# Optimization experiments

Measured on AMD Instinct MI355X. Metric: run time of the kernel, lower is better.

The kernel has to match this reference:

```python
import jax, jax.numpy as jnp
import numpy as np

N, E, G = 50000, 800000, 64   # nodes, edges, graphs
IN, HID, H = 128, 64, 4       # in_channels, hidden_channels, heads


def setup_inputs() -> dict:
    key = jax.random.key(0)
    ks = jax.random.split(key, 32)
    r = lambda i, shape, sc=0.05: jax.random.normal(ks[i], shape, jnp.float32) * sc
    inp = {
        "x": jax.random.normal(ks[0], (N, IN), jnp.float32),
        "edge_index": jax.random.randint(ks[1], (2, E), 0, N),
        "batch": jnp.sort(jax.random.randint(ks[2], (N,), 0, G)),
        # GATConv 1: in -> hidden, heads=4, concat
        "W1": r(3, (IN, H * HID)), "a_src1": r(4, (H, HID)), "a_dst1": r(5, (H, HID)), "b1": r(6, (H * HID,)),
        "bn1_g": 1.0 + r(7, (H * HID,)), "bn1_b": r(8, (H * HID,)), "bn1_m": r(9, (H * HID,)),
        "bn1_v": jax.random.uniform(ks[10], (H * HID,), jnp.float32, 0.5, 1.5),
        # GATConv 2: hidden*heads -> hidden, heads=4, concat
        "W2": r(11, (H * HID, H * HID)), "a_src2": r(12, (H, HID)), "a_dst2": r(13, (H, HID)), "b2": r(14, (H * HID,)),
        "bn2_g": 1.0 + r(15, (H * HID,)), "bn2_b": r(16, (H * HID,)), "bn2_m": r(17, (H * HID,)),
        "bn2_v": jax.random.uniform(ks[18], (H * HID,), jnp.float32, 0.5, 1.5),
        # GATConv 3: hidden*heads -> hidden, heads=1
        "W3": r(19, (H * HID, HID)), "a_src3": r(20, (1, HID)), "a_dst3": r(21, (1, HID)), "b3": r(22, (HID,)),
        # projection MLP: Linear(2*hidden, hidden) -> ReLU -> Linear(hidden, hidden)
        "P1": r(23, (2 * HID, HID)), "pb1": r(24, (HID,)),
        "P2": r(25, (HID, HID)), "pb2": r(26, (HID,)),
    }
    return inp


def _gat_conv(x, src, dst, n, W, a_s, a_d, b, concat):
    """PyG-style GATConv (eval mode). src/dst already include self-loops."""
    Hh, C = a_s.shape
    h = (x @ W).reshape(n, Hh, C)                       # [N, H, C]
    al_s = jnp.einsum('nhc,hc->nh', h, a_s)             # [N, H]
    al_d = jnp.einsum('nhc,hc->nh', h, a_d)             # [N, H]
    e = jax.nn.leaky_relu(al_s[src] + al_d[dst], 0.2)   # [E', H]
    # segment softmax over incoming edges of each dst node
    m = jax.ops.segment_max(e, dst, num_segments=n)     # [N, H] (finite: self-loops)
    ex = jnp.exp(e - m[dst])
    den = jax.ops.segment_sum(ex, dst, num_segments=n)
    alpha = ex / den[dst]                               # [E', H]
    out = jax.ops.segment_sum(h[src] * alpha[..., None], dst, num_segments=n)  # [N, H, C]
    out = out.reshape(n, Hh * C) if concat else out.mean(axis=1)
    return out + b


def _bn(x, g, b, m, v):
    return (x - m) * jax.lax.rsqrt(v + 1e-5) * g + b


def _forward(x, edge_index, batch,
             W1, a_src1, a_dst1, b1, bn1_g, bn1_b, bn1_m, bn1_v,
             W2, a_src2, a_dst2, b2, bn2_g, bn2_b, bn2_m, bn2_v,
             W3, a_src3, a_dst3, b3, P1, pb1, P2, pb2):
    n = x.shape[0]
    loop = jnp.arange(n)
    src = jnp.concatenate([edge_index[0], loop])        # add_self_loops=True
    dst = jnp.concatenate([edge_index[1], loop])
    h = _gat_conv(x, src, dst, n, W1, a_src1, a_dst1, b1, True)
    h = jax.nn.elu(_bn(h, bn1_g, bn1_b, bn1_m, bn1_v))  # dropout inactive in eval
    h = _gat_conv(h, src, dst, n, W2, a_src2, a_dst2, b2, True)
    h = jax.nn.elu(_bn(h, bn2_g, bn2_b, bn2_m, bn2_v))
    h = _gat_conv(h, src, dst, n, W3, a_src3, a_dst3, b3, False)  # heads=1
    x_max = jax.ops.segment_max(h, batch, num_segments=G)
    cnt = jax.ops.segment_sum(jnp.ones((n, 1), h.dtype), batch, num_segments=G)
    x_mean = jax.ops.segment_sum(h, batch, num_segments=G) / jnp.maximum(cnt, 1.0)
    z = jnp.concatenate([x_max, x_mean], axis=1)        # [G, 2*HID]
    z = jax.nn.relu(z @ P1 + pb1)
    return z @ P2 + pb2                                  # [G, HID]


def reference(x, edge_index, batch,
              W1, a_src1, a_dst1, b1, bn1_g, bn1_b, bn1_m, bn1_v,
              W2, a_src2, a_dst2, b2, bn2_g, bn2_b, bn2_m, bn2_v,
              W3, a_src3, a_dst3, b3, P1, pb1, P2, pb2):
    return _forward(x, edge_index, batch,
                    W1, a_src1, a_dst1, b1, bn1_g, bn1_b, bn1_m, bn1_v,
                    W2, a_src2, a_dst2, b2, bn2_g, bn2_b, bn2_m, bn2_v,
                    W3, a_src3, a_dst3, b3, P1, pb1, P2, pb2)
```

## Files before the change

kernel.cpp:

```cpp
#include <hip/hip_runtime.h>

typedef unsigned int uint;
typedef unsigned short ushort;

#define NFIX 50000
#define EFIX 800000
#define GFIX 64
#define BCAP 64
#define DCAP 128
#define WSTRIDE 136
#define PSL 16

__device__ __forceinline__ float bflo(uint u) { return __uint_as_float(u << 16); }
__device__ __forceinline__ float bfhi(uint u) { return __uint_as_float(u & 0xffff0000u); }
__device__ __forceinline__ float bf1(ushort u) { return __uint_as_float(((uint)u) << 16); }
__device__ __forceinline__ ushort f2bf(float f) {
    uint u = __float_as_uint(f);
    u += 0x7fffu + ((u >> 16) & 1u);
    return (ushort)(u >> 16);
}
__device__ __forceinline__ float lrelu(float x) { return fmaxf(x, 0.2f * x); }

typedef __attribute__((ext_vector_type(8))) short bf16x8;
typedef __attribute__((ext_vector_type(4))) float f32x4;
union U16B { uint4 u; bf16x8 v; };

__global__ void detect_idx_width(const int* __restrict__ ei, int* __restrict__ flag) {
    const int lane = threadIdx.x & 63;
    int v = (lane < 16) ? ei[2 * lane + 1] : 0;
    unsigned long long any = __ballot(v != 0);
    if (lane == 0 && blockIdx.x == 0) *flag = (any == 0ULL) ? 1 : 0;
}

__device__ __forceinline__ int ld_idx(const int* __restrict__ p, long i, int w64) {
    return w64 ? p[2 * i] : p[i];
}

__global__ void count_scatter(const int* __restrict__ ei, const int* __restrict__ flag,
                              int* __restrict__ cnt, int* __restrict__ ssb) {
    const int w64 = *flag;
    int e = blockIdx.x * 256 + threadIdx.x;
    if (e < EFIX) {
        int d = ld_idx(ei, (long)EFIX + e, w64);
        int s = ld_idx(ei, e, w64);
        int slot = atomicAdd(&cnt[d], 1);
        if (slot < BCAP) ssb[d * BCAP + slot] = s;
    }
}

#define XCNT 1600000
#define T1 (XCNT)
#define T2 (T1 + 128 * 256)
#define T3 (T2 + 256 * 256)
#define T4 (T3 + 256 * 64)
__global__ void prep(const float* __restrict__ x, ushort* __restrict__ xbf,
                     const float* __restrict__ W1, ushort* __restrict__ Wt1,
                     const float* __restrict__ W2, ushort* __restrict__ Wt2,
                     const float* __restrict__ W3, ushort* __restrict__ Wt3) {
    int i = blockIdx.x * 256 + threadIdx.x;
    if (i < XCNT) {
        int idx = i * 4;
        float4 v = *(const float4*)(x + idx);
        ushort4 o; o.x = f2bf(v.x); o.y = f2bf(v.y); o.z = f2bf(v.z); o.w = f2bf(v.w);
        *(ushort4*)(xbf + idx) = o;
    } else if (i < T2) {
        int j = i - T1; int k = j >> 8, c = j & 255;
        Wt1[c * 128 + k] = f2bf(W1[j]);
    } else if (i < T3) {
        int j = i - T2; int k = j >> 8, c = j & 255;
        Wt2[c * 256 + k] = f2bf(W2[j]);
    } else if (i < T4) {
        int j = i - T3; int k = j >> 6, c = j & 63;
        Wt3[c * 256 + k] = f2bf(W3[j]);
    }
}

template <int K>
__global__ __launch_bounds__(256) void gemm_mfma_nc256(const ushort* __restrict__ X,
                                                       const ushort* __restrict__ Wt,
                                                       const float* __restrict__ as_,
                                                       const float* __restrict__ ad_,
                                                       ushort* __restrict__ Hout,
                                                       float* __restrict__ als,
                                                       float* __restrict__ ald, int M) {
    const int wave = threadIdx.x >> 6;
    const int lane = threadIdx.x & 63;
    const int rowBase = blockIdx.x * 64;
    const int colBase = wave * 64;
    const int tr = lane & 15;
    const int kq = (lane >> 4) * 8;

    f32x4 acc[4][4];
#pragma unroll
    for (int i = 0; i < 4; ++i)
#pragma unroll
        for (int j = 0; j < 4; ++j) acc[i][j] = (f32x4){0.f, 0.f, 0.f, 0.f};

    const ushort* ap[4];
    const ushort* bp[4];
#pragma unroll
    for (int mi = 0; mi < 4; ++mi) {
        int r = rowBase + mi * 16 + tr;
        r = r < M ? r : M - 1;
        ap[mi] = X + (size_t)r * K + kq;
    }
#pragma unroll
    for (int ni = 0; ni < 4; ++ni)
        bp[ni] = Wt + (size_t)(colBase + ni * 16 + tr) * K + kq;

    for (int k0 = 0; k0 < K; k0 += 32) {
        bf16x8 a[4], b[4];
#pragma unroll
        for (int mi = 0; mi < 4; ++mi) { U16B t; t.u = *(const uint4*)(ap[mi] + k0); a[mi] = t.v; }
#pragma unroll
        for (int ni = 0; ni < 4; ++ni) { U16B t; t.u = *(const uint4*)(bp[ni] + k0); b[ni] = t.v; }
#pragma unroll
        for (int mi = 0; mi < 4; ++mi)
#pragma unroll
            for (int ni = 0; ni < 4; ++ni)
                acc[mi][ni] = __builtin_amdgcn_mfma_f32_16x16x32_bf16(a[mi], b[ni], acc[mi][ni], 0, 0, 0);
    }

    const int orow = (lane >> 4) * 4;
    const int ocol = colBase + tr;
#pragma unroll
    for (int mi = 0; mi < 4; ++mi) {
#pragma unroll
        for (int r = 0; r < 4; ++r) {
            int row = rowBase + mi * 16 + orow + r;
            if (row < M) {
#pragma unroll
                for (int ni = 0; ni < 4; ++ni)
                    Hout[(size_t)row * 256 + ocol + ni * 16] = f2bf(acc[mi][ni][r]);
            }
        }
    }

    float asv[4], adv[4];
#pragma unroll
    for (int ni = 0; ni < 4; ++ni) {
        asv[ni] = as_[wave * 64 + ni * 16 + tr];
        adv[ni] = ad_[wave * 64 + ni * 16 + tr];
    }
#pragma unroll
    for (int mi = 0; mi < 4; ++mi) {
#pragma unroll
        for (int r = 0; r < 4; ++r) {
            float ps = acc[mi][0][r] * asv[0] + acc[mi][1][r] * asv[1]
                     + acc[mi][2][r] * asv[2] + acc[mi][3][r] * asv[3];
            float pd = acc[mi][0][r] * adv[0] + acc[mi][1][r] * adv[1]
                     + acc[mi][2][r] * adv[2] + acc[mi][3][r] * adv[3];
#pragma unroll
            for (int off = 1; off < 16; off <<= 1) {
                ps += __shfl_xor(ps, off, 64);
                pd += __shfl_xor(pd, off, 64);
            }
            int row = rowBase + mi * 16 + orow + r;
            if (tr == 0 && row < M) {
                als[(size_t)row * 4 + wave] = ps;
                ald[(size_t)row * 4 + wave] = pd;
            }
        }
    }
}

template <int K, int NC, int HAL>
__global__ __launch_bounds__(256) void gemm_mfma(const ushort* __restrict__ X,
                                                 const ushort* __restrict__ Wt,
                                                 const float* __restrict__ as_,
                                                 const float* __restrict__ ad_,
                                                 ushort* __restrict__ Hout,
                                                 float* __restrict__ als,
                                                 float* __restrict__ ald, int M) {
    const int wave = threadIdx.x >> 6;
    const int lane = threadIdx.x & 63;
    const int rowBase = blockIdx.x * 256 + wave * 64;
    const int head = blockIdx.y;
    const int colBase = head * 64;
    const int tr = lane & 15;
    const int kq = (lane >> 4) * 8;

    f32x4 acc[4][4];
#pragma unroll
    for (int i = 0; i < 4; ++i)
#pragma unroll
        for (int j = 0; j < 4; ++j) acc[i][j] = (f32x4){0.f, 0.f, 0.f, 0.f};

    const ushort* ap[4];
    const ushort* bp[4];
#pragma unroll
    for (int mi = 0; mi < 4; ++mi) {
        int r = rowBase + mi * 16 + tr;
        r = r < M ? r : M - 1;
        ap[mi] = X + (size_t)r * K + kq;
    }
#pragma unroll
    for (int ni = 0; ni < 4; ++ni)
        bp[ni] = Wt + (size_t)(colBase + ni * 16 + tr) * K + kq;

    for (int k0 = 0; k0 < K; k0 += 32) {
        bf16x8 a[4], b[4];
#pragma unroll
        for (int mi = 0; mi < 4; ++mi) { U16B t; t.u = *(const uint4*)(ap[mi] + k0); a[mi] = t.v; }
#pragma unroll
        for (int ni = 0; ni < 4; ++ni) { U16B t; t.u = *(const uint4*)(bp[ni] + k0); b[ni] = t.v; }
#pragma unroll
        for (int mi = 0; mi < 4; ++mi)
#pragma unroll
            for (int ni = 0; ni < 4; ++ni)
                acc[mi][ni] = __builtin_amdgcn_mfma_f32_16x16x32_bf16(a[mi], b[ni], acc[mi][ni], 0, 0, 0);
    }

    const int orow = (lane >> 4) * 4;
    const int ocol = colBase + tr;
#pragma unroll
    for (int mi = 0; mi < 4; ++mi) {
#pragma unroll
        for (int r = 0; r < 4; ++r) {
            int row = rowBase + mi * 16 + orow + r;
            if (row < M) {
#pragma unroll
                for (int ni = 0; ni < 4; ++ni)
                    Hout[(size_t)row * NC + ocol + ni * 16] = f2bf(acc[mi][ni][r]);
            }
        }
    }

    float asv[4], adv[4];
#pragma unroll
    for (int ni = 0; ni < 4; ++ni) {
        asv[ni] = as_[head * 64 + ni * 16 + tr];
        adv[ni] = ad_[head * 64 + ni * 16 + tr];
    }
#pragma unroll
    for (int mi = 0; mi < 4; ++mi) {
#pragma unroll
        for (int r = 0; r < 4; ++r) {
            float ps = acc[mi][0][r] * asv[0] + acc[mi][1][r] * asv[1]
                     + acc[mi][2][r] * asv[2] + acc[mi][3][r] * asv[3];
            float pd = acc[mi][0][r] * adv[0] + acc[mi][1][r] * adv[1]
                     + acc[mi][2][r] * adv[2] + acc[mi][3][r] * adv[3];
#pragma unroll
            for (int off = 1; off < 16; off <<= 1) {
                ps += __shfl_xor(ps, off, 64);
                pd += __shfl_xor(pd, off, 64);
            }
            int row = rowBase + mi * 16 + orow + r;
            if (tr == 0 && row < M) {
                als[(size_t)row * HAL + head] = ps;
                ald[(size_t)row * HAL + head] = pd;
            }
        }
    }
}

template <int H_, int C, bool FINAL>
__global__ __launch_bounds__(256) void gat_gather(
    const ushort* __restrict__ hb, const float* __restrict__ als, const float* __restrict__ ald,
    const int* __restrict__ cnt, const int* __restrict__ ssb,
    const float* __restrict__ bias, const float* __restrict__ bng, const float* __restrict__ bnb,
    const float* __restrict__ bnm, const float* __restrict__ bnv,
    ushort* __restrict__ xnext, float* __restrict__ yout, int n) {
    constexpr int TC = H_ * C;
    constexpr int CPL = TC / 64;
    constexpr int GW = 64 / H_;
    constexpr int KMAX = DCAP / GW;
    constexpr int SHIFT = (TC == 256) ? 8 : 6;
    __shared__ float s_w[4][H_ * WSTRIDE];
    __shared__ int s_idx[4][DCAP];
    const int wv = threadIdx.x >> 6;
    const int node = blockIdx.x * 4 + wv;
    if (node >= n) return;
    const int lane = threadIdx.x & 63;
    const int head = lane / GW;
    const int hl = lane & (GW - 1);
    const int c0 = lane * CPL;

    const float aldn = ald[(size_t)node * H_ + head];
    const float selfle = lrelu(als[(size_t)node * H_ + head] + aldn);
    const int e0 = node * BCAP;
    int d = cnt[node];
    d = d < BCAP ? d : BCAP;

    float acc[CPL];

    {
        float le_reg[KMAX];
        int s_reg[KMAX];
        float m = selfle;
#pragma unroll
        for (int k = 0; k < KMAX; ++k) {
            int j = hl + k * GW;
            if (j < d) {
                int s = ssb[e0 + j];
                s_reg[k] = s;
                float le = lrelu(als[(size_t)s * H_ + head] + aldn);
                le_reg[k] = le;
                m = fmaxf(m, le);
            }
        }
#pragma unroll
        for (int off = 1; off < GW; off <<= 1) m = fmaxf(m, __shfl_xor(m, off, 64));

        float dsum = (hl == 0) ? __expf(selfle - m) : 0.f;
#pragma unroll
        for (int k = 0; k < KMAX; ++k) {
            int j = hl + k * GW;
            if (j < d) {
                float p = __expf(le_reg[k] - m);
                dsum += p;
                s_w[wv][head * WSTRIDE + j] = p;
                if (head == 0) s_idx[wv][j] = s_reg[k] << SHIFT;
            }
        }
#pragma unroll
        for (int off = 1; off < GW; off <<= 1) dsum += __shfl_xor(dsum, off, 64);
        const float inv = 1.0f / dsum;

        {
            float psf = __expf(selfle - m);
            if constexpr (CPL == 4) {
                uint2 hu = *(const uint2*)(hb + (size_t)node * TC + c0);
                acc[0] = psf * bflo(hu.x); acc[1] = psf * bfhi(hu.x);
                acc[2] = psf * bflo(hu.y); acc[3] = psf * bfhi(hu.y);
            } else {
                acc[0] = psf * bf1(hb[(size_t)node * TC + c0]);
            }
        }
        const float* wbase = &s_w[wv][head * WSTRIDE];
        const int* ibase = &s_idx[wv][0];
        const ushort* hc = hb + c0;
        int j = 0;
        for (; j + 8 <= d; j += 8) {
            float4 wa = *(const float4*)(wbase + j);
            float4 wb2 = *(const float4*)(wbase + j + 4);
            int4 ia = *(const int4*)(ibase + j);
            int4 ib = *(const int4*)(ibase + j + 4);
            if constexpr (CPL == 4) {
                uint2 h0 = *(const uint2*)(hc + ia.x);
                uint2 h1 = *(const uint2*)(hc + ia.y);
                uint2 h2 = *(const uint2*)(hc + ia.z);
                uint2 h3 = *(const uint2*)(hc + ia.w);
                uint2 h4 = *(const uint2*)(hc + ib.x);
                uint2 h5 = *(const uint2*)(hc + ib.y);
                uint2 h6 = *(const uint2*)(hc + ib.z);
                uint2 h7 = *(const uint2*)(hc + ib.w);
                acc[0] = fmaf(wa.x, bflo(h0.x), acc[0]); acc[1] = fmaf(wa.x, bfhi(h0.x), acc[1]);
                acc[2] = fmaf(wa.x, bflo(h0.y), acc[2]); acc[3] = fmaf(wa.x, bfhi(h0.y), acc[3]);
                acc[0] = fmaf(wa.y, bflo(h1.x), acc[0]); acc[1] = fmaf(wa.y, bfhi(h1.x), acc[1]);
                acc[2] = fmaf(wa.y, bflo(h1.y), acc[2]); acc[3] = fmaf(wa.y, bfhi(h1.y), acc[3]);
                acc[0] = fmaf(wa.z, bflo(h2.x), acc[0]); acc[1] = fmaf(wa.z, bfhi(h2.x), acc[1]);
                acc[2] = fmaf(wa.z, bflo(h2.y), acc[2]); acc[3] = fmaf(wa.z, bfhi(h2.y), acc[3]);
                acc[0] = fmaf(wa.w, bflo(h3.x), acc[0]); acc[1] = fmaf(wa.w, bfhi(h3.x), acc[1]);
                acc[2] = fmaf(wa.w, bflo(h3.y), acc[2]); acc[3] = fmaf(wa.w, bfhi(h3.y), acc[3]);
                acc[0] = fmaf(wb2.x, bflo(h4.x), acc[0]); acc[1] = fmaf(wb2.x, bfhi(h4.x), acc[1]);
                acc[2] = fmaf(wb2.x, bflo(h4.y), acc[2]); acc[3] = fmaf(wb2.x, bfhi(h4.y), acc[3]);
                acc[0] = fmaf(wb2.y, bflo(h5.x), acc[0]); acc[1] = fmaf(wb2.y, bfhi(h5.x), acc[1]);
                acc[2] = fmaf(wb2.y, bflo(h5.y), acc[2]); acc[3] = fmaf(wb2.y, bfhi(h5.y), acc[3]);
                acc[0] = fmaf(wb2.z, bflo(h6.x), acc[0]); acc[1] = fmaf(wb2.z, bfhi(h6.x), acc[1]);
                acc[2] = fmaf(wb2.z, bflo(h6.y), acc[2]); acc[3] = fmaf(wb2.z, bfhi(h6.y), acc[3]);
                acc[0] = fmaf(wb2.w, bflo(h7.x), acc[0]); acc[1] = fmaf(wb2.w, bfhi(h7.x), acc[1]);
                acc[2] = fmaf(wb2.w, bflo(h7.y), acc[2]); acc[3] = fmaf(wb2.w, bfhi(h7.y), acc[3]);
            } else {
                float h0 = bf1(hc[ia.x]), h1 = bf1(hc[ia.y]), h2 = bf1(hc[ia.z]), h3 = bf1(hc[ia.w]);
                float h4 = bf1(hc[ib.x]), h5 = bf1(hc[ib.y]), h6 = bf1(hc[ib.z]), h7 = bf1(hc[ib.w]);
                acc[0] = fmaf(wa.x, h0, acc[0]); acc[0] = fmaf(wa.y, h1, acc[0]);
                acc[0] = fmaf(wa.z, h2, acc[0]); acc[0] = fmaf(wa.w, h3, acc[0]);
                acc[0] = fmaf(wb2.x, h4, acc[0]); acc[0] = fmaf(wb2.y, h5, acc[0]);
                acc[0] = fmaf(wb2.z, h6, acc[0]); acc[0] = fmaf(wb2.w, h7, acc[0]);
            }
        }
        for (; j + 4 <= d; j += 4) {
            float4 wa = *(const float4*)(wbase + j);
            int4 ia = *(const int4*)(ibase + j);
            if constexpr (CPL == 4) {
                uint2 h0 = *(const uint2*)(hc + ia.x);
                uint2 h1 = *(const uint2*)(hc + ia.y);
                uint2 h2 = *(const uint2*)(hc + ia.z);
                uint2 h3 = *(const uint2*)(hc + ia.w);
                acc[0] = fmaf(wa.x, bflo(h0.x), acc[0]); acc[1] = fmaf(wa.x, bfhi(h0.x), acc[1]);
                acc[2] = fmaf(wa.x, bflo(h0.y), acc[2]); acc[3] = fmaf(wa.x, bfhi(h0.y), acc[3]);
                acc[0] = fmaf(wa.y, bflo(h1.x), acc[0]); acc[1] = fmaf(wa.y, bfhi(h1.x), acc[1]);
                acc[2] = fmaf(wa.y, bflo(h1.y), acc[2]); acc[3] = fmaf(wa.y, bfhi(h1.y), acc[3]);
                acc[0] = fmaf(wa.z, bflo(h2.x), acc[0]); acc[1] = fmaf(wa.z, bfhi(h2.x), acc[1]);
                acc[2] = fmaf(wa.z, bflo(h2.y), acc[2]); acc[3] = fmaf(wa.z, bfhi(h2.y), acc[3]);
                acc[0] = fmaf(wa.w, bflo(h3.x), acc[0]); acc[1] = fmaf(wa.w, bfhi(h3.x), acc[1]);
                acc[2] = fmaf(wa.w, bflo(h3.y), acc[2]); acc[3] = fmaf(wa.w, bfhi(h3.y), acc[3]);
            } else {
                float h0 = bf1(hc[ia.x]), h1 = bf1(hc[ia.y]), h2 = bf1(hc[ia.z]), h3 = bf1(hc[ia.w]);
                acc[0] = fmaf(wa.x, h0, acc[0]); acc[0] = fmaf(wa.y, h1, acc[0]);
                acc[0] = fmaf(wa.z, h2, acc[0]); acc[0] = fmaf(wa.w, h3, acc[0]);
            }
        }
        for (; j < d; ++j) {
            float w = wbase[j];
            int io = ibase[j];
            if constexpr (CPL == 4) {
                uint2 hu = *(const uint2*)(hc + io);
                acc[0] = fmaf(w, bflo(hu.x), acc[0]); acc[1] = fmaf(w, bfhi(hu.x), acc[1]);
                acc[2] = fmaf(w, bflo(hu.y), acc[2]); acc[3] = fmaf(w, bfhi(hu.y), acc[3]);
            } else {
                acc[0] = fmaf(w, bf1(hc[io]), acc[0]);
            }
        }
#pragma unroll
        for (int q = 0; q < CPL; ++q) acc[q] *= inv;
    }

    if constexpr (!FINAL) {
        float4 bi = *(const float4*)(bias + c0);
        float4 gg = *(const float4*)(bng + c0);
        float4 bb = *(const float4*)(bnb + c0);
        float4 mm = *(const float4*)(bnm + c0);
        float4 vv = *(const float4*)(bnv + c0);
        float biA[4] = { bi.x, bi.y, bi.z, bi.w };
        float ggA[4] = { gg.x, gg.y, gg.z, gg.w };
        float bbA[4] = { bb.x, bb.y, bb.z, bb.w };
        float mmA[4] = { mm.x, mm.y, mm.z, mm.w };
        float vvA[4] = { vv.x, vv.y, vv.z, vv.w };
        float r[4];
#pragma unroll
        for (int j2 = 0; j2 < 4; ++j2) {
            float v = acc[j2] + biA[j2];
            v = (v - mmA[j2]) * rsqrtf(vvA[j2] + 1e-5f) * ggA[j2] + bbA[j2];
            v = v > 0.f ? v : (__expf(v) - 1.0f);
            r[j2] = v;
        }
        uint p0 = (uint)f2bf(r[0]) | ((uint)f2bf(r[1]) << 16);
        uint p1 = (uint)f2bf(r[2]) | ((uint)f2bf(r[3]) << 16);
        uint2 o; o.x = p0; o.y = p1;
        *(uint2*)(xnext + (size_t)node * TC + c0) = o;
    } else {
        yout[(size_t)node * TC + c0] = acc[0] + bias[c0];
    }
}

__device__ __forceinline__ int lbound_w(const int* a, int n, int v, int w64) {
    int lo = 0, hi = n;
    while (lo < hi) {
        int mid = (lo + hi) >> 1;
        int bv = w64 ? a[2 * mid] : a[mid];
        if (bv < v) lo = mid + 1; else hi = mid;
    }
    return lo;
}

__global__ __launch_bounds__(256) void pool_part(const float* __restrict__ y, const int* __restrict__ batch,
                                                 const int* __restrict__ flag,
                                                 float* __restrict__ part) {
    const int w64 = *flag;
    const int g = blockIdx.x;
    const int sl = blockIdx.y;
    const int t = threadIdx.x;
    const int start = lbound_w(batch, NFIX, g, w64);
    const int end = lbound_w(batch, NFIX, g + 1, w64);
    const int len = end - start;
    const int s0 = start + (int)((long)len * sl / PSL);
    const int s1 = start + (int)((long)len * (sl + 1) / PSL);
    const int ch = t & 63, sub = t >> 6;
    float mx = -3.0e38f, sm = 0.f;
    for (int i = s0 + sub; i < s1; i += 4) {
        float v = y[(size_t)i * 64 + ch];
        mx = fmaxf(mx, v); sm += v;
    }
    __shared__ float smx[256], ssm[256];
    smx[t] = mx; ssm[t] = sm;
    __syncthreads();
    if (t < 64) {
        mx = fmaxf(fmaxf(smx[t], smx[t + 64]), fmaxf(smx[t + 128], smx[t + 192]));
        sm = ssm[t] + ssm[t + 64] + ssm[t + 128] + ssm[t + 192];
        float* pb = part + ((size_t)g * PSL + sl) * 128;
        pb[t] = mx;
        pb[64 + t] = sm;
    }
}

__global__ __launch_bounds__(64) void pool_fin_mlp(const float* __restrict__ part,
                                                   const int* __restrict__ batch,
                                                   const int* __restrict__ flag,
                                                   const float* __restrict__ P1, const float* __restrict__ pb1,
                                                   const float* __restrict__ P2, const float* __restrict__ pb2,
                                                   float* __restrict__ out) {
    const int w64 = *flag;
    const int g = blockIdx.x;
    const int t = threadIdx.x;
    const int start = lbound_w(batch, NFIX, g, w64);
    const int end = lbound_w(batch, NFIX, g + 1, w64);
    const int cnt = end - start;
    __shared__ float pl[128];
    __shared__ float z[64];
    float mx = -3.0e38f, sm = 0.f;
    const float* pb = part + (size_t)g * PSL * 128;
#pragma unroll
    for (int s = 0; s < PSL; ++s) {
        mx = fmaxf(mx, pb[s * 128 + t]);
        sm += pb[s * 128 + 64 + t];
    }
    float mean = cnt > 0 ? sm / (float)cnt : 0.f;
    if (cnt == 0) mx = 0.f;
    pl[t] = mx;
    pl[64 + t] = mean;
    __syncthreads();
    float a = pb1[t];
    for (int k = 0; k < 128; ++k) a = fmaf(pl[k], P1[k * 64 + t], a);
    z[t] = fmaxf(a, 0.f);
    __syncthreads();
    float o = pb2[t];
    for (int k = 0; k < 64; ++k) o = fmaf(z[k], P2[k * 64 + t], o);
    out[(size_t)g * 64 + t] = o;
}

__global__ void write_code(float* out, float code) {
    if (threadIdx.x == 0 && blockIdx.x == 0) out[0] = code;
}

extern "C" void kernel_launch(void* const* d_in, const int* in_sizes, int n_in,
                              void* d_out, int out_size, void* d_ws, size_t ws_size,
                              hipStream_t stream) {
    const float* x = (const float*)d_in[0];
    const int* ei = (const int*)d_in[1];
    const int* batch = (const int*)d_in[2];
    const float* W1 = (const float*)d_in[3];
    const float* as1 = (const float*)d_in[4];
    const float* ad1 = (const float*)d_in[5];
    const float* b1 = (const float*)d_in[6];
    const float* bn1g = (const float*)d_in[7];
    const float* bn1b = (const float*)d_in[8];
    const float* bn1m = (const float*)d_in[9];
    const float* bn1v = (const float*)d_in[10];
    const float* W2 = (const float*)d_in[11];
    const float* as2 = (const float*)d_in[12];
    const float* ad2 = (const float*)d_in[13];
    const float* b2 = (const float*)d_in[14];
    const float* bn2g = (const float*)d_in[15];
    const float* bn2b = (const float*)d_in[16];
    const float* bn2m = (const float*)d_in[17];
    const float* bn2v = (const float*)d_in[18];
    const float* W3 = (const float*)d_in[19];
    const float* as3 = (const float*)d_in[20];
    const float* ad3 = (const float*)d_in[21];
    const float* b3 = (const float*)d_in[22];
    const float* P1 = (const float*)d_in[23];
    const float* pb1 = (const float*)d_in[24];
    const float* P2 = (const float*)d_in[25];
    const float* pb2 = (const float*)d_in[26];
    float* out = (float*)d_out;
    (void)n_in; (void)out_size; (void)in_sizes;

    const int N_ = NFIX;
    const int E_ = EFIX;

    char* ws = (char*)d_ws;
    size_t off = 0;
    auto alloc = [&](size_t bytes) -> void* {
        void* p = ws + off;
        off = (off + bytes + 255) & ~(size_t)255;
        return p;
    };
    ushort* hbuf = (ushort*)alloc((size_t)N_ * 256 * 2);
    ushort* xbuf = (ushort*)alloc((size_t)N_ * 256 * 2);
    float* als = (float*)alloc((size_t)N_ * 4 * 4);
    float* ald = (float*)alloc((size_t)N_ * 4 * 4);
    int* cnt = (int*)alloc((size_t)N_ * 4);
    int* ssb = (int*)alloc((size_t)N_ * BCAP * 4);
    ushort* Wt1 = (ushort*)alloc(128 * 256 * 2);
    ushort* Wt2 = (ushort*)alloc(256 * 256 * 2);
    ushort* Wt3 = (ushort*)alloc(256 * 64 * 2);
    float* part = (float*)alloc((size_t)GFIX * PSL * 128 * 4);
    int* flag = (int*)alloc(256);
    ushort* xbf = xbuf;
    float* y3 = (float*)xbuf;
    const size_t needed = off;

    if (ws_size < needed) {
        write_code<<<1, 64, 0, stream>>>(out, 1000.0f + (float)(needed >> 20));
        return;
    }

    const int eg = (E_ + 255) / 256;
    const int ng4 = (N_ + 3) / 4;
    const int rb = (N_ + 255) / 256;
    const int rb64 = (N_ + 63) / 64;

    detect_idx_width<<<1, 64, 0, stream>>>(ei, flag);
    hipMemsetAsync(cnt, 0, (size_t)N_ * 4, stream);
    count_scatter<<<eg, 256, 0, stream>>>(ei, flag, cnt, ssb);

    prep<<<(T4 + 255) / 256, 256, 0, stream>>>(x, xbf, W1, Wt1, W2, Wt2, W3, Wt3);

    gemm_mfma_nc256<128><<<rb64, 256, 0, stream>>>(xbf, Wt1, as1, ad1, hbuf, als, ald, N_);
    gat_gather<4, 64, false><<<ng4, 256, 0, stream>>>(hbuf, als, ald, cnt, ssb,
                                                      b1, bn1g, bn1b, bn1m, bn1v, xbuf, nullptr, N_);
    gemm_mfma_nc256<256><<<rb64, 256, 0, stream>>>(xbuf, Wt2, as2, ad2, hbuf, als, ald, N_);
    gat_gather<4, 64, false><<<ng4, 256, 0, stream>>>(hbuf, als, ald, cnt, ssb,
                                                      b2, bn2g, bn2b, bn2m, bn2v, xbuf, nullptr, N_);
    gemm_mfma<256, 64, 1><<<dim3(rb, 1), 256, 0, stream>>>(xbuf, Wt3, as3, ad3, hbuf, als, ald, N_);
    gat_gather<1, 64, true><<<ng4, 256, 0, stream>>>(hbuf, als, ald, cnt, ssb,
                                                     b3, nullptr, nullptr, nullptr, nullptr,
                                                     nullptr, y3, N_);

    pool_part<<<dim3(GFIX, PSL), 256, 0, stream>>>(y3, batch, flag, part);
    pool_fin_mlp<<<GFIX, 64, 0, stream>>>(part, batch, flag, P1, pb1, P2, pb2, out);
}
```

Measured before the change: 434.1 us.

## Split GAT gather into softmax-weight kernel and channel-sliced gather kernel

Each GAT layer's fused softmax+gather kernel is split in two. A weights kernel computes normalized attention coefficients per edge and head into a global buffer. A slice kernel launches a grid over 32-channel slices and nodes, with two half-waves interleaving edges and combining through a shuffle. The aim is more parallelism and cache locality per channel slice, at the cost of an extra launch, a global weight write/read, and narrow 2-byte scattered loads instead of 8-byte vector loads.

```diff
diff --git a/kernel.cpp b/kernel.cpp
--- a/kernel.cpp
+++ b/kernel.cpp
@@ -7,8 +7,6 @@
 #define EFIX 800000
 #define GFIX 64
 #define BCAP 64
-#define DCAP 128
-#define WSTRIDE 136
 #define PSL 16
 
 __device__ __forceinline__ float bflo(uint u) { return __uint_as_float(u << 16); }
@@ -254,27 +252,19 @@
     }
 }
 
-template <int H_, int C, bool FINAL>
-__global__ __launch_bounds__(256) void gat_gather(
-    const ushort* __restrict__ hb, const float* __restrict__ als, const float* __restrict__ ald,
+template <int H_>
+__global__ __launch_bounds__(256) void gat_weights(
+    const float* __restrict__ als, const float* __restrict__ ald,
     const int* __restrict__ cnt, const int* __restrict__ ssb,
-    const float* __restrict__ bias, const float* __restrict__ bng, const float* __restrict__ bnb,
-    const float* __restrict__ bnm, const float* __restrict__ bnv,
-    ushort* __restrict__ xnext, float* __restrict__ yout, int n) {
-    constexpr int TC = H_ * C;
-    constexpr int CPL = TC / 64;
+    float* __restrict__ wbuf, float* __restrict__ wself, int n) {
     constexpr int GW = 64 / H_;
-    constexpr int KMAX = DCAP / GW;
-    constexpr int SHIFT = (TC == 256) ? 8 : 6;
-    __shared__ float s_w[4][H_ * WSTRIDE];
-    __shared__ int s_idx[4][DCAP];
+    constexpr int KMAX = BCAP / GW;
     const int wv = threadIdx.x >> 6;
     const int node = blockIdx.x * 4 + wv;
     if (node >= n) return;
     const int lane = threadIdx.x & 63;
     const int head = lane / GW;
     const int hl = lane & (GW - 1);
-    const int c0 = lane * CPL;
 
     const float aldn = ald[(size_t)node * H_ + head];
     const float selfle = lrelu(als[(size_t)node * H_ + head] + aldn);
@@ -282,156 +272,119 @@
     int d = cnt[node];
     d = d < BCAP ? d : BCAP;
 
-    float acc[CPL];
-
-    {
-        float le_reg[KMAX];
-        int s_reg[KMAX];
-        float m = selfle;
-#pragma unroll
-        for (int k = 0; k < KMAX; ++k) {
-            int j = hl + k * GW;
-            if (j < d) {
-                int s = ssb[e0 + j];
-                s_reg[k] = s;
-                float le = lrelu(als[(size_t)s * H_ + head] + aldn);
-                le_reg[k] = le;
-                m = fmaxf(m, le);
-            }
-        }
-#pragma unroll
-        for (int off = 1; off < GW; off <<= 1) m = fmaxf(m, __shfl_xor(m, off, 64));
-
-        float dsum = (hl == 0) ? __expf(selfle - m) : 0.f;
-#pragma unroll
-        for (int k = 0; k < KMAX; ++k) {
-            int j = hl + k * GW;
-            if (j < d) {
-                float p = __expf(le_reg[k] - m);
-                dsum += p;
-                s_w[wv][head * WSTRIDE + j] = p;
-                if (head == 0) s_idx[wv][j] = s_reg[k] << SHIFT;
-            }
-        }
-#pragma unroll
-        for (int off = 1; off < GW; off <<= 1) dsum += __shfl_xor(dsum, off, 64);
-        const float inv = 1.0f / dsum;
-
-        {
-            float psf = __expf(selfle - m);
-            if constexpr (CPL == 4) {
-                uint2 hu = *(const uint2*)(hb + (size_t)node * TC + c0);
-                acc[0] = psf * bflo(hu.x); acc[1] = psf * bfhi(hu.x);
-                acc[2] = psf * bflo(hu.y); acc[3] = psf * bfhi(hu.y);
-            } else {
-                acc[0] = psf * bf1(hb[(size_t)node * TC + c0]);
-            }
-        }
-        const float* wbase = &s_w[wv][head * WSTRIDE];
-        const int* ibase = &s_idx[wv][0];
-        const ushort* hc = hb + c0;
-        int j = 0;
-        for (; j + 8 <= d; j += 8) {
-            float4 wa = *(const float4*)(wbase + j);
-            float4 wb2 = *(const float4*)(wbase + j + 4);
-            int4 ia = *(const int4*)(ibase + j);
-            int4 ib = *(const int4*)(ibase + j + 4);
-            if constexpr (CPL == 4) {
-                uint2 h0 = *(const uint2*)(hc + ia.x);
-                uint2 h1 = *(const uint2*)(hc + ia.y);
-                uint2 h2 = *(const uint2*)(hc + ia.z);
-                uint2 h3 = *(const uint2*)(hc + ia.w);
-                uint2 h4 = *(const uint2*)(hc + ib.x);
-                uint2 h5 = *(const uint2*)(hc + ib.y);
-                uint2 h6 = *(const uint2*)(hc + ib.z);
-                uint2 h7 = *(const uint2*)(hc + ib.w);
-                acc[0] = fmaf(wa.x, bflo(h0.x), acc[0]); acc[1] = fmaf(wa.x, bfhi(h0.x), acc[1]);
-                acc[2] = fmaf(wa.x, bflo(h0.y), acc[2]); acc[3] = fmaf(wa.x, bfhi(h0.y), acc[3]);
-                acc[0] = fmaf(wa.y, bflo(h1.x), acc[0]); acc[1] = fmaf(wa.y, bfhi(h1.x), acc[1]);
-                acc[2] = fmaf(wa.y, bflo(h1.y), acc[2]); acc[3] = fmaf(wa.y, bfhi(h1.y), acc[3]);
-                acc[0] = fmaf(wa.z, bflo(h2.x), acc[0]); acc[1] = fmaf(wa.z, bfhi(h2.x), acc[1]);
-                acc[2] = fmaf(wa.z, bflo(h2.y), acc[2]); acc[3] = fmaf(wa.z, bfhi(h2.y), acc[3]);
-                acc[0] = fmaf(wa.w, bflo(h3.x), acc[0]); acc[1] = fmaf(wa.w, bfhi(h3.x), acc[1]);
-                acc[2] = fmaf(wa.w, bflo(h3.y), acc[2]); acc[3] = fmaf(wa.w, bfhi(h3.y), acc[3]);
-                acc[0] = fmaf(wb2.x, bflo(h4.x), acc[0]); acc[1] = fmaf(wb2.x, bfhi(h4.x), acc[1]);
-                acc[2] = fmaf(wb2.x, bflo(h4.y), acc[2]); acc[3] = fmaf(wb2.x, bfhi(h4.y), acc[3]);
-                acc[0] = fmaf(wb2.y, bflo(h5.x), acc[0]); acc[1] = fmaf(wb2.y, bfhi(h5.x), acc[1]);
-                acc[2] = fmaf(wb2.y, bflo(h5.y), acc[2]); acc[3] = fmaf(wb2.y, bfhi(h5.y), acc[3]);
-                acc[0] = fmaf(wb2.z, bflo(h6.x), acc[0]); acc[1] = fmaf(wb2.z, bfhi(h6.x), acc[1]);
-                acc[2] = fmaf(wb2.z, bflo(h6.y), acc[2]); acc[3] = fmaf(wb2.z, bfhi(h6.y), acc[3]);
-                acc[0] = fmaf(wb2.w, bflo(h7.x), acc[0]); acc[1] = fmaf(wb2.w, bfhi(h7.x), acc[1]);
-                acc[2] = fmaf(wb2.w, bflo(h7.y), acc[2]); acc[3] = fmaf(wb2.w, bfhi(h7.y), acc[3]);
-            } else {
-                float h0 = bf1(hc[ia.x]), h1 = bf1(hc[ia.y]), h2 = bf1(hc[ia.z]), h3 = bf1(hc[ia.w]);
-                float h4 = bf1(hc[ib.x]), h5 = bf1(hc[ib.y]), h6 = bf1(hc[ib.z]), h7 = bf1(hc[ib.w]);
-                acc[0] = fmaf(wa.x, h0, acc[0]); acc[0] = fmaf(wa.y, h1, acc[0]);
-                acc[0] = fmaf(wa.z, h2, acc[0]); acc[0] = fmaf(wa.w, h3, acc[0]);
-                acc[0] = fmaf(wb2.x, h4, acc[0]); acc[0] = fmaf(wb2.y, h5, acc[0]);
-                acc[0] = fmaf(wb2.z, h6, acc[0]); acc[0] = fmaf(wb2.w, h7, acc[0]);
-            }
-        }
-        for (; j + 4 <= d; j += 4) {
-            float4 wa = *(const float4*)(wbase + j);
-            int4 ia = *(const int4*)(ibase + j);
-            if constexpr (CPL == 4) {
-                uint2 h0 = *(const uint2*)(hc + ia.x);
-                uint2 h1 = *(const uint2*)(hc + ia.y);
-                uint2 h2 = *(const uint2*)(hc + ia.z);
-                uint2 h3 = *(const uint2*)(hc + ia.w);
-                acc[0] = fmaf(wa.x, bflo(h0.x), acc[0]); acc[1] = fmaf(wa.x, bfhi(h0.x), acc[1]);
-                acc[2] = fmaf(wa.x, bflo(h0.y), acc[2]); acc[3] = fmaf(wa.x, bfhi(h0.y), acc[3]);
-                acc[0] = fmaf(wa.y, bflo(h1.x), acc[0]); acc[1] = fmaf(wa.y, bfhi(h1.x), acc[1]);
-                acc[2] = fmaf(wa.y, bflo(h1.y), acc[2]); acc[3] = fmaf(wa.y, bfhi(h1.y), acc[3]);
-                acc[0] = fmaf(wa.z, bflo(h2.x), acc[0]); acc[1] = fmaf(wa.z, bfhi(h2.x), acc[1]);
-                acc[2] = fmaf(wa.z, bflo(h2.y), acc[2]); acc[3] = fmaf(wa.z, bfhi(h2.y), acc[3]);
-                acc[0] = fmaf(wa.w, bflo(h3.x), acc[0]); acc[1] = fmaf(wa.w, bfhi(h3.x), acc[1]);
-                acc[2] = fmaf(wa.w, bflo(h3.y), acc[2]); acc[3] = fmaf(wa.w, bfhi(h3.y), acc[3]);
-            } else {
-                float h0 = bf1(hc[ia.x]), h1 = bf1(hc[ia.y]), h2 = bf1(hc[ia.z]), h3 = bf1(hc[ia.w]);
-                acc[0] = fmaf(wa.x, h0, acc[0]); acc[0] = fmaf(wa.y, h1, acc[0]);
-                acc[0] = fmaf(wa.z, h2, acc[0]); acc[0] = fmaf(wa.w, h3, acc[0]);
-            }
-        }
-        for (; j < d; ++j) {
-            float w = wbase[j];
-            int io = ibase[j];
-            if constexpr (CPL == 4) {
-                uint2 hu = *(const uint2*)(hc + io);
-                acc[0] = fmaf(w, bflo(hu.x), acc[0]); acc[1] = fmaf(w, bfhi(hu.x), acc[1]);
-                acc[2] = fmaf(w, bflo(hu.y), acc[2]); acc[3] = fmaf(w, bfhi(hu.y), acc[3]);
-            } else {
-                acc[0] = fmaf(w, bf1(hc[io]), acc[0]);
-            }
-        }
-#pragma unroll
-        for (int q = 0; q < CPL; ++q) acc[q] *= inv;
-    }
-
-    if constexpr (!FINAL) {
-        float4 bi = *(const float4*)(bias + c0);
-        float4 gg = *(const float4*)(bng + c0);
-        float4 bb = *(const float4*)(bnb + c0);
-        float4 mm = *(const float4*)(bnm + c0);
-        float4 vv = *(const float4*)(bnv + c0);
-        float biA[4] = { bi.x, bi.y, bi.z, bi.w };
-        float ggA[4] = { gg.x, gg.y, gg.z, gg.w };
-        float bbA[4] = { bb.x, bb.y, bb.z, bb.w };
-        float mmA[4] = { mm.x, mm.y, mm.z, mm.w };
-        float vvA[4] = { vv.x, vv.y, vv.z, vv.w };
-        float r[4];
-#pragma unroll
-        for (int j2 = 0; j2 < 4; ++j2) {
-            float v = acc[j2] + biA[j2];
-            v = (v - mmA[j2]) * rsqrtf(vvA[j2] + 1e-5f) * ggA[j2] + bbA[j2];
+    float le_reg[KMAX];
+    float m = selfle;
+#pragma unroll
+    for (int k = 0; k < KMAX; ++k) {
+        int j = hl + k * GW;
+        if (j < d) {
+            int s = ssb[e0 + j];
+            float le = lrelu(als[(size_t)s * H_ + head] + aldn);
+            le_reg[k] = le;
+            m = fmaxf(m, le);
+        }
+    }
+#pragma unroll
+    for (int off = 1; off < GW; off <<= 1) m = fmaxf(m, __shfl_xor(m, off, 64));
+
+    float p_reg[KMAX];
+    float dsum = (hl == 0) ? __expf(selfle - m) : 0.f;
+#pragma unroll
+    for (int k = 0; k < KMAX; ++k) {
+        int j = hl + k * GW;
+        if (j < d) {
+            float p = __expf(le_reg[k] - m);
+            p_reg[k] = p;
+            dsum += p;
+        }
+    }
+#pragma unroll
+    for (int off = 1; off < GW; off <<= 1) dsum += __shfl_xor(dsum, off, 64);
+    const float inv = 1.0f / dsum;
+
+    float* wp = wbuf + (size_t)head * (NFIX * BCAP) + e0;
+#pragma unroll
+    for (int k = 0; k < KMAX; ++k) {
+        int j = hl + k * GW;
+        if (j < d) wp[j] = p_reg[k] * inv;
+    }
+    if (hl == 0) wself[(size_t)node * H_ + head] = __expf(selfle - m) * inv;
+}
+
+template <int H_, bool FINAL>
+__global__ __launch_bounds__(256) void gat_gather_slice(
+    const ushort* __restrict__ hb,
+    const int* __restrict__ cnt, const int* __restrict__ ssb,
+    const float* __restrict__ wbuf, const float* __restrict__ wself,
+    const float* __restrict__ bias, const float* __restrict__ bng, const float* __restrict__ bnb,
+    const float* __restrict__ bnm, const float* __restrict__ bnv,
+    ushort* __restrict__ xnext, float* __restrict__ yout, int n) {
+    constexpr int TC = H_ * 64;
+    const int wv = threadIdx.x >> 6;
+    const int node = blockIdx.y * 4 + wv;
+    if (node >= n) return;
+    const int lane = threadIdx.x & 63;
+    const int s = blockIdx.x;
+    const int chBase = s * 32;
+    const int head = chBase >> 6;
+    const int half = lane >> 5;
+    const int ch = chBase + (lane & 31);
+
+    const int e0 = node * BCAP;
+    int d = cnt[node];
+    d = d < BCAP ? d : BCAP;
+    const int* ib = ssb + e0;
+    const float* wb = wbuf + (size_t)head * (NFIX * BCAP) + e0;
+
+    float acc = (half == 0) ? wself[(size_t)node * H_ + head] * bf1(hb[(size_t)node * TC + ch])
+                            : 0.0f;
+
+    int j = half;
+    for (; j + 14 < d; j += 16) {
+        int i0 = ib[j], i1 = ib[j + 2], i2 = ib[j + 4], i3 = ib[j + 6];
+        int i4 = ib[j + 8], i5 = ib[j + 10], i6 = ib[j + 12], i7 = ib[j + 14];
+        float w0 = wb[j], w1 = wb[j + 2], w2 = wb[j + 4], w3 = wb[j + 6];
+        float w4 = wb[j + 8], w5 = wb[j + 10], w6 = wb[j + 12], w7 = wb[j + 14];
+        float h0 = bf1(hb[(size_t)i0 * TC + ch]);
+        float h1 = bf1(hb[(size_t)i1 * TC + ch]);
+        float h2 = bf1(hb[(size_t)i2 * TC + ch]);
+        float h3 = bf1(hb[(size_t)i3 * TC + ch]);
+        float h4 = bf1(hb[(size_t)i4 * TC + ch]);
+        float h5 = bf1(hb[(size_t)i5 * TC + ch]);
+        float h6 = bf1(hb[(size_t)i6 * TC + ch]);
+        float h7 = bf1(hb[(size_t)i7 * TC + ch]);
+        acc = fmaf(w0, h0, acc); acc = fmaf(w1, h1, acc);
+        acc = fmaf(w2, h2, acc); acc = fmaf(w3, h3, acc);
+        acc = fmaf(w4, h4, acc); acc = fmaf(w5, h5, acc);
+        acc = fmaf(w6, h6, acc); acc = fmaf(w7, h7, acc);
+    }
+    for (; j + 6 < d; j += 8) {
+        int i0 = ib[j], i1 = ib[j + 2], i2 = ib[j + 4], i3 = ib[j + 6];
+        float w0 = wb[j], w1 = wb[j + 2], w2 = wb[j + 4], w3 = wb[j + 6];
+        float h0 = bf1(hb[(size_t)i0 * TC + ch]);
+        float h1 = bf1(hb[(size_t)i1 * TC + ch]);
+        float h2 = bf1(hb[(size_t)i2 * TC + ch]);
+        float h3 = bf1(hb[(size_t)i3 * TC + ch]);
+        acc = fmaf(w0, h0, acc); acc = fmaf(w1, h1, acc);
+        acc = fmaf(w2, h2, acc); acc = fmaf(w3, h3, acc);
+    }
+    for (; j < d; j += 2) {
+        int i0 = ib[j];
+        float w0 = wb[j];
+        acc = fmaf(w0, bf1(hb[(size_t)i0 * TC + ch]), acc);
+    }
+
+    acc += __shfl_xor(acc, 32, 64);
+
+    if (half == 0) {
+        if constexpr (!FINAL) {
+            float v = acc + bias[ch];
+            v = (v - bnm[ch]) * rsqrtf(bnv[ch] + 1e-5f) * bng[ch] + bnb[ch];
             v = v > 0.f ? v : (__expf(v) - 1.0f);
-            r[j2] = v;
-        }
-        uint p0 = (uint)f2bf(r[0]) | ((uint)f2bf(r[1]) << 16);
-        uint p1 = (uint)f2bf(r[2]) | ((uint)f2bf(r[3]) << 16);
-        uint2 o; o.x = p0; o.y = p1;
-        *(uint2*)(xnext + (size_t)node * TC + c0) = o;
-    } else {
-        yout[(size_t)node * TC + c0] = acc[0] + bias[c0];
+            xnext[(size_t)node * TC + ch] = f2bf(v);
+        } else {
+            yout[(size_t)node * 64 + ch] = acc + bias[ch];
+        }
     }
 }
 
@@ -563,6 +516,8 @@
     float* ald = (float*)alloc((size_t)N_ * 4 * 4);
     int* cnt = (int*)alloc((size_t)N_ * 4);
     int* ssb = (int*)alloc((size_t)N_ * BCAP * 4);
+    float* wbuf = (float*)alloc((size_t)4 * N_ * BCAP * 4);
+    float* wself = (float*)alloc((size_t)N_ * 4 * 4);
     ushort* Wt1 = (ushort*)alloc(128 * 256 * 2);
     ushort* Wt2 = (ushort*)alloc(256 * 256 * 2);
     ushort* Wt3 = (ushort*)alloc(256 * 64 * 2);
@@ -589,15 +544,20 @@
     prep<<<(T4 + 255) / 256, 256, 0, stream>>>(x, xbf, W1, Wt1, W2, Wt2, W3, Wt3);
 
     gemm_mfma_nc256<128><<<rb64, 256, 0, stream>>>(xbf, Wt1, as1, ad1, hbuf, als, ald, N_);
-    gat_gather<4, 64, false><<<ng4, 256, 0, stream>>>(hbuf, als, ald, cnt, ssb,
-                                                      b1, bn1g, bn1b, bn1m, bn1v, xbuf, nullptr, N_);
+    gat_weights<4><<<ng4, 256, 0, stream>>>(als, ald, cnt, ssb, wbuf, wself, N_);
+    gat_gather_slice<4, false><<<dim3(8, ng4), 256, 0, stream>>>(hbuf, cnt, ssb, wbuf, wself,
+                                                                 b1, bn1g, bn1b, bn1m, bn1v,
+                                                                 xbuf, nullptr, N_);
     gemm_mfma_nc256<256><<<rb64, 256, 0, stream>>>(xbuf, Wt2, as2, ad2, hbuf, als, ald, N_);
-    gat_gather<4, 64, false><<<ng4, 256, 0, stream>>>(hbuf, als, ald, cnt, ssb,
-                                                      b2, bn2g, bn2b, bn2m, bn2v, xbuf, nullptr, N_);
+    gat_weights<4><<<ng4, 256, 0, stream>>>(als, ald, cnt, ssb, wbuf, wself, N_);
+    gat_gather_slice<4, false><<<dim3(8, ng4), 256, 0, stream>>>(hbuf, cnt, ssb, wbuf, wself,
+                                                                 b2, bn2g, bn2b, bn2m, bn2v,
+                                                                 xbuf, nullptr, N_);
     gemm_mfma<256, 64, 1><<<dim3(rb, 1), 256, 0, stream>>>(xbuf, Wt3, as3, ad3, hbuf, als, ald, N_);
-    gat_gather<1, 64, true><<<ng4, 256, 0, stream>>>(hbuf, als, ald, cnt, ssb,
-                                                     b3, nullptr, nullptr, nullptr, nullptr,
-                                                     nullptr, y3, N_);
+    gat_weights<1><<<ng4, 256, 0, stream>>>(als, ald, cnt, ssb, wbuf, wself, N_);
+    gat_gather_slice<1, true><<<dim3(2, ng4), 256, 0, stream>>>(hbuf, cnt, ssb, wbuf, wself,
+                                                                b3, nullptr, nullptr, nullptr, nullptr,
+                                                                nullptr, y3, N_);
 
     pool_part<<<dim3(GFIX, PSL), 256, 0, stream>>>(y3, batch, flag, part);
     pool_fin_mlp<<<GFIX, 64, 0, stream>>>(part, batch, flag, P1, pb1, P2, pb2, out);
```

New measurement: 736.3 us. +69.6%, slower.
